# Optimization experiments

Measured on AMD Instinct MI355X. Metric: run time of the kernel, lower is better.

Reference implementation:

```python
import jax, jax.numpy as jnp
import numpy as np
import math

N = 100000      # num vertices
M = 50000       # num hyperedges
NNZ = 800000    # incidence entries
F_IN = 128
NHID = 128
NCLS = 40
DEPTH = 4
ALPHA = 0.1     # restart_alpha
LAMDA = 0.5


def setup_inputs() -> dict:
    key = jax.random.key(0)
    ks = jax.random.split(key, 8)
    x = jax.random.normal(ks[0], (N, F_IN), jnp.float32)
    vertex = jax.random.randint(ks[1], (NNZ,), 0, N)
    edges = jax.random.randint(ks[2], (NNZ,), 0, M)
    s0 = 1.0 / np.sqrt(F_IN)
    sh = 1.0 / np.sqrt(NHID)
    W0 = jax.random.uniform(ks[3], (F_IN, NHID), jnp.float32, -s0, s0)
    b0 = jax.random.uniform(ks[4], (NHID,), jnp.float32, -s0, s0)
    Ws = jax.random.uniform(ks[5], (DEPTH, NHID, NHID), jnp.float32, -sh, sh)
    Wout = jax.random.uniform(ks[6], (NHID, NCLS), jnp.float32, -sh, sh)
    bout = jax.random.uniform(ks[7], (NCLS,), jnp.float32, -sh, sh)
    return {"x": x, "W0": W0, "b0": b0, "Ws": Ws, "Wout": Wout,
            "bout": bout, "vertex": vertex, "edges": edges}


def reference(x, W0, b0, Ws, Wout, bout, vertex, edges):
    ones = jnp.ones((NNZ, 1), x.dtype)
    cnt_e = jnp.maximum(jax.ops.segment_sum(ones, edges, num_segments=M), 1.0)
    cnt_v = jnp.maximum(jax.ops.segment_sum(ones, vertex, num_segments=N), 1.0)

    x = jax.nn.relu(x @ W0 + b0)
    x0 = x
    for i in range(DEPTH):
        beta = math.log(LAMDA / (i + 1) + 1.0)
        # vertex -> edge mean aggregation
        Xve = x[vertex]                                          # [NNZ, NHID]
        Xe = jax.ops.segment_sum(Xve, edges, num_segments=M) / cnt_e
        # edge -> vertex mean aggregation
        Xev = Xe[edges]                                          # [NNZ, NHID]
        Xv = jax.ops.segment_sum(Xev, vertex, num_segments=N) / cnt_v
        # L2 row-normalize with detached scale (use_norm=True)
        norm = jnp.linalg.norm(Xv, axis=1, keepdims=True)
        scale = jax.lax.stop_gradient(jnp.where(norm > 0, 1.0 / norm, 0.0))
        Xv = Xv * scale
        # alpha/beta residual blend (UniGCNII)
        Xi = (1.0 - ALPHA) * Xv + ALPHA * x0
        x = jax.nn.relu((1.0 - beta) * Xi + beta * (Xi @ Ws[i]))
    return x @ Wout + bout
```

## Files before the change

### kernel.cpp

```cpp
#include <hip/hip_runtime.h>

#define NV 100000
#define NE 50000
#define NNZ_C 800000
#define CAP_E 64
#define CAP_V 48
#define NB_E 391
#define NB_V 782
#define CAPB_E 2560
#define CAPB_V 1408
#define OVF_CAP 810000
#define T_ITEMS 4096
#define N_TILES ((NNZ_C + T_ITEMS - 1) / T_ITEMS)

typedef unsigned int uint32;
typedef unsigned short u16;
typedef u16 u16x8 __attribute__((ext_vector_type(8)));
typedef short short8 __attribute__((ext_vector_type(8)));
typedef float floatx16 __attribute__((ext_vector_type(16)));

__device__ __forceinline__ float bf2f(u16 h) {
  return __uint_as_float(((uint32)h) << 16);
}
__device__ __forceinline__ u16 f2bf(float f) {
  uint32 u = __float_as_uint(f);
  u += 0x7FFF + ((u >> 16) & 1);
  return (u16)(u >> 16);
}


__global__ void zero_misc(int* __restrict__ cur, int n,
                          u16* __restrict__ dummyX, u16* __restrict__ dummyXe) {
  int i = blockIdx.x * blockDim.x + threadIdx.x;
  if (i < n) cur[i] = 0;
  if (i < 128) { dummyX[i] = 0; dummyXe[i] = 0; }
}


__global__ __launch_bounds__(256) void scatter_binned(const int* __restrict__ vertex,
                                                      const int* __restrict__ edges,
                                                      int* __restrict__ curE,
                                                      int* __restrict__ curV,
                                                      int* __restrict__ ovfCnt,
                                                      uint32* __restrict__ pairE,
                                                      uint32* __restrict__ pairV,
                                                      uint2* __restrict__ ovfE,
                                                      uint2* __restrict__ ovfV) {
  __shared__ int histE[NB_E], baseE[NB_E];
  __shared__ int histV[NB_V], baseV[NB_V];
  int t = threadIdx.x;
  for (int tile = blockIdx.x; tile < N_TILES; tile += gridDim.x) {
    for (int b = t; b < NB_E; b += 256) histE[b] = 0;
    for (int b = t; b < NB_V; b += 256) histV[b] = 0;
    __syncthreads();
    int base = tile * T_ITEMS;
    int ev[16], vv[16], rE[16], rV[16];
    #pragma unroll
    for (int i = 0; i < 16; i++) {
      int k = base + t + i * 256;
      if (k < NNZ_C) {
        ev[i] = edges[k];
        vv[i] = vertex[k];
        rE[i] = atomicAdd(&histE[ev[i] >> 7], 1);
        rV[i] = atomicAdd(&histV[vv[i] >> 7], 1);
      }
    }
    __syncthreads();
    for (int b = t; b < NB_E; b += 256) {
      int h = histE[b];
      baseE[b] = h ? atomicAdd(&curE[b], h) : 0;
    }
    for (int b = t; b < NB_V; b += 256) {
      int h = histV[b];
      baseV[b] = h ? atomicAdd(&curV[b], h) : 0;
    }
    __syncthreads();
    #pragma unroll
    for (int i = 0; i < 16; i++) {
      int k = base + t + i * 256;
      if (k < NNZ_C) {
        uint32 e = (uint32)ev[i], v = (uint32)vv[i];
        uint32 pkE = ((e & 127u) << 25) | v;
        uint32 pkV = ((v & 127u) << 25) | e;
        int pE = baseE[e >> 7] + rE[i];
        if (pE < CAPB_E) pairE[(size_t)(e >> 7) * CAPB_E + pE] = pkE;
        else { int op = atomicAdd(&ovfCnt[0], 1); if (op < OVF_CAP) ovfE[op] = make_uint2(e >> 7, pkE); }
        int pV = baseV[v >> 7] + rV[i];
        if (pV < CAPB_V) pairV[(size_t)(v >> 7) * CAPB_V + pV] = pkV;
        else { int op = atomicAdd(&ovfCnt[1], 1); if (op < OVF_CAP) ovfV[op] = make_uint2(v >> 7, pkV); }
      }
    }
    __syncthreads();
  }
}

__global__ __launch_bounds__(256) void expand(const uint32* __restrict__ pairs,
                                              const int* __restrict__ cur, int capb,
                                              const uint2* __restrict__ ovf,
                                              const int* __restrict__ ovfCnt,
                                              int* __restrict__ items, int cap,
                                              int* __restrict__ cnt, int nKeys,
                                              int P, int dummy) {
  __shared__ int lcnt[128];
  int b = blockIdx.x, t = threadIdx.x;
  if (t < 128) lcnt[t] = 0;
  __syncthreads();
  int n = min(cur[b], capb);
  const uint32* p = pairs + (size_t)b * capb;
  for (int i = t; i < n; i += 256) {
    uint32 w = p[i];
    int loc = w >> 25;
    int val = (int)(w & 0x1FFFFFFu);
    int r = atomicAdd(&lcnt[loc], 1);
    if (r < cap) items[(size_t)((b << 7) + loc) * cap + r] = val;
  }
  int novf = min(*ovfCnt, OVF_CAP);
  for (int i = t; i < novf; i += 256) {
    uint2 w = ovf[i];
    if ((int)w.x == b) {
      int loc = w.y >> 25;
      int val = (int)(w.y & 0x1FFFFFFu);
      int r = atomicAdd(&lcnt[loc], 1);
      if (r < cap) items[(size_t)((b << 7) + loc) * cap + r] = val;
    }
  }
  __syncthreads();
  if (t < 128) {
    int key = (b << 7) + t;
    if (key < nKeys) {
      int c = lcnt[t];
      cnt[key] = c;
      int cc = min(c, cap);
      int padded = min((cc + P - 1) & ~(P - 1), cap);
      for (int r = cc; r < padded; r++)
        items[(size_t)key * cap + r] = dummy;
    }
  }
}


__global__ void prep_weights(const float* __restrict__ W0, const float* __restrict__ Ws,
                             u16* __restrict__ WT) {
  int idx = blockIdx.x * blockDim.x + threadIdx.x;
  if (idx >= 5 * 16384) return;
  const float betas[4] = {0.4054651081f, 0.2231435513f, 0.1541506798f, 0.1177830357f};
  int sec = idx >> 14;
  int rc = idx & 16383;
  int n = rc >> 7, k = rc & 127;
  float v;
  if (sec == 0) {
    v = W0[k * 128 + n];
  } else {
    int i = sec - 1;
    float b = betas[i];
    v = b * Ws[i * 16384 + k * 128 + n];
    if (k == n) v += 1.0f - b;
  }
  WT[idx] = f2bf(v);
}


__global__ __launch_bounds__(256) void edge_agg(const u16* __restrict__ Xh,
                                                const int* __restrict__ cntE,
                                                const int* __restrict__ itemsE,
                                                u16* __restrict__ Xeh) {
  int g = threadIdx.x >> 4;
  int lane = threadIdx.x & 15;
  int e = blockIdx.x * 16 + g;
  int cnt = cntE[e];
  int n16 = (min(cnt, CAP_E) + 15) & ~15;
  const int* it = itemsE + (size_t)e * CAP_E;
  float acc[8] = {0.f, 0.f, 0.f, 0.f, 0.f, 0.f, 0.f, 0.f};
  for (int j = 0; j < n16; j += 16) {
    int4 i0 = *(const int4*)(it + j);
    int4 i1 = *(const int4*)(it + j + 4);
    int4 i2 = *(const int4*)(it + j + 8);
    int4 i3 = *(const int4*)(it + j + 12);
    u16x8 r0 = *(const u16x8*)(Xh + (size_t)i0.x * 128 + lane * 8);
    u16x8 r1 = *(const u16x8*)(Xh + (size_t)i0.y * 128 + lane * 8);
    u16x8 r2 = *(const u16x8*)(Xh + (size_t)i0.z * 128 + lane * 8);
    u16x8 r3 = *(const u16x8*)(Xh + (size_t)i0.w * 128 + lane * 8);
    u16x8 r4 = *(const u16x8*)(Xh + (size_t)i1.x * 128 + lane * 8);
    u16x8 r5 = *(const u16x8*)(Xh + (size_t)i1.y * 128 + lane * 8);
    u16x8 r6 = *(const u16x8*)(Xh + (size_t)i1.z * 128 + lane * 8);
    u16x8 r7 = *(const u16x8*)(Xh + (size_t)i1.w * 128 + lane * 8);
    u16x8 r8 = *(const u16x8*)(Xh + (size_t)i2.x * 128 + lane * 8);
    u16x8 r9 = *(const u16x8*)(Xh + (size_t)i2.y * 128 + lane * 8);
    u16x8 rA = *(const u16x8*)(Xh + (size_t)i2.z * 128 + lane * 8);
    u16x8 rB = *(const u16x8*)(Xh + (size_t)i2.w * 128 + lane * 8);
    u16x8 rC = *(const u16x8*)(Xh + (size_t)i3.x * 128 + lane * 8);
    u16x8 rD = *(const u16x8*)(Xh + (size_t)i3.y * 128 + lane * 8);
    u16x8 rE = *(const u16x8*)(Xh + (size_t)i3.z * 128 + lane * 8);
    u16x8 rF = *(const u16x8*)(Xh + (size_t)i3.w * 128 + lane * 8);
    #pragma unroll
    for (int q = 0; q < 8; q++) {
      float s0 = (bf2f(r0[q]) + bf2f(r1[q])) + (bf2f(r2[q]) + bf2f(r3[q]));
      float s1 = (bf2f(r4[q]) + bf2f(r5[q])) + (bf2f(r6[q]) + bf2f(r7[q]));
      float s2 = (bf2f(r8[q]) + bf2f(r9[q])) + (bf2f(rA[q]) + bf2f(rB[q]));
      float s3 = (bf2f(rC[q]) + bf2f(rD[q])) + (bf2f(rE[q]) + bf2f(rF[q]));
      acc[q] += (s0 + s1) + (s2 + s3);
    }
  }
  float inv = 1.f / fmaxf((float)cnt, 1.f);
  u16x8 o;
  #pragma unroll
  for (int q = 0; q < 8; q++) o[q] = f2bf(acc[q] * inv);
  *(u16x8*)(Xeh + (size_t)e * 128 + lane * 8) = o;
}

__global__ __launch_bounds__(256) void vertex_agg(const u16* __restrict__ Xeh,
                                                  const int* __restrict__ cntV,
                                                  const int* __restrict__ itemsV,
                                                  const u16* __restrict__ x0h,
                                                  u16* __restrict__ Xih) {
  int g = threadIdx.x >> 4;
  int lane = threadIdx.x & 15;
  int v = blockIdx.x * 16 + g;
  int cnt = cntV[v];
  int n8 = (min(cnt, CAP_V) + 7) & ~7;
  const int* it = itemsV + (size_t)v * CAP_V;
  u16x8 x0v = *(const u16x8*)(x0h + (size_t)v * 128 + lane * 8);
  float acc[8] = {0.f, 0.f, 0.f, 0.f, 0.f, 0.f, 0.f, 0.f};
  for (int j = 0; j < n8; j += 8) {
    int4 e0 = *(const int4*)(it + j);
    int4 e1 = *(const int4*)(it + j + 4);
    u16x8 r0 = *(const u16x8*)(Xeh + (size_t)e0.x * 128 + lane * 8);
    u16x8 r1 = *(const u16x8*)(Xeh + (size_t)e0.y * 128 + lane * 8);
    u16x8 r2 = *(const u16x8*)(Xeh + (size_t)e0.z * 128 + lane * 8);
    u16x8 r3 = *(const u16x8*)(Xeh + (size_t)e0.w * 128 + lane * 8);
    u16x8 r4 = *(const u16x8*)(Xeh + (size_t)e1.x * 128 + lane * 8);
    u16x8 r5 = *(const u16x8*)(Xeh + (size_t)e1.y * 128 + lane * 8);
    u16x8 r6 = *(const u16x8*)(Xeh + (size_t)e1.z * 128 + lane * 8);
    u16x8 r7 = *(const u16x8*)(Xeh + (size_t)e1.w * 128 + lane * 8);
    #pragma unroll
    for (int q = 0; q < 8; q++)
      acc[q] += ((bf2f(r0[q]) + bf2f(r1[q])) + (bf2f(r2[q]) + bf2f(r3[q]))) +
                ((bf2f(r4[q]) + bf2f(r5[q])) + (bf2f(r6[q]) + bf2f(r7[q])));
  }
  float inv = 1.f / fmaxf((float)cnt, 1.f);
  float sq = 0.f;
  #pragma unroll
  for (int q = 0; q < 8; q++) { acc[q] *= inv; sq += acc[q] * acc[q]; }
  sq += __shfl_xor(sq, 1, 64);
  sq += __shfl_xor(sq, 2, 64);
  sq += __shfl_xor(sq, 4, 64);
  sq += __shfl_xor(sq, 8, 64);
  float scale = (sq > 0.f) ? rsqrtf(sq) : 0.f;
  u16x8 o;
  #pragma unroll
  for (int q = 0; q < 8; q++)
    o[q] = f2bf(0.9f * acc[q] * scale + 0.1f * bf2f(x0v[q]));
  *(u16x8*)(Xih + (size_t)v * 128 + lane * 8) = o;
}


__global__ __launch_bounds__(256, 4) void gemm_mfma(const u16* __restrict__ Ah,
                                                    const u16* __restrict__ WT,
                                                    u16* __restrict__ Yh, int nrows) {
  __shared__ u16 As[128 * 136];
  int t = threadIdx.x;
  int row0 = blockIdx.x * 128;
  #pragma unroll
  for (int i = 0; i < 8; i++) {
    int idx = t + 256 * i;
    int r = idx >> 4, c8 = idx & 15;
    u16x8 v = {0, 0, 0, 0, 0, 0, 0, 0};
    if (row0 + r < nrows) v = *(const u16x8*)(Ah + (size_t)(row0 + r) * 128 + c8 * 8);
    *(u16x8*)&As[r * 136 + c8 * 8] = v;
  }
  __syncthreads();

  int w = t >> 6, lane = t & 63;
  int l31 = lane & 31, kh = lane >> 5;
  int wr = w >> 1, wc = w & 1;
  floatx16 acc[2][2];
  #pragma unroll
  for (int rt = 0; rt < 2; rt++)
    #pragma unroll
    for (int ct = 0; ct < 2; ct++)
      #pragma unroll
      for (int q = 0; q < 16; q++) acc[rt][ct][q] = 0.f;

  const u16* wtb0 = WT + (size_t)(wc * 64 + l31) * 128;
  const u16* wtb1 = WT + (size_t)(wc * 64 + 32 + l31) * 128;
  #pragma unroll
  for (int ks = 0; ks < 8; ks++) {
    int koff = ks * 16 + kh * 8;
    short8 b0 = *(const short8*)(wtb0 + koff);
    short8 b1 = *(const short8*)(wtb1 + koff);
    short8 a0 = *(const short8*)&As[(wr * 64 + l31) * 136 + koff];
    short8 a1 = *(const short8*)&As[(wr * 64 + 32 + l31) * 136 + koff];
    acc[0][0] = __builtin_amdgcn_mfma_f32_32x32x16_bf16(a0, b0, acc[0][0], 0, 0, 0);
    acc[0][1] = __builtin_amdgcn_mfma_f32_32x32x16_bf16(a0, b1, acc[0][1], 0, 0, 0);
    acc[1][0] = __builtin_amdgcn_mfma_f32_32x32x16_bf16(a1, b0, acc[1][0], 0, 0, 0);
    acc[1][1] = __builtin_amdgcn_mfma_f32_32x32x16_bf16(a1, b1, acc[1][1], 0, 0, 0);
  }
  __syncthreads();

  #pragma unroll
  for (int rt = 0; rt < 2; rt++)
    #pragma unroll
    for (int ct = 0; ct < 2; ct++) {
      int col = wc * 64 + ct * 32 + l31;
      #pragma unroll
      for (int reg = 0; reg < 16; reg++) {
        int row = wr * 64 + rt * 32 + (reg & 3) + 8 * (reg >> 2) + 4 * kh;
        As[row * 136 + col] = f2bf(fmaxf(acc[rt][ct][reg], 0.f));
      }
    }
  __syncthreads();
  #pragma unroll
  for (int i = 0; i < 8; i++) {
    int idx = t + 256 * i;
    int r = idx >> 4, c8 = idx & 15;
    if (row0 + r < nrows)
      *(u16x8*)(Yh + (size_t)(row0 + r) * 128 + c8 * 8) =
          *(const u16x8*)&As[r * 136 + c8 * 8];
  }
}

__global__ __launch_bounds__(256, 4) void gemm_first(const float* __restrict__ A,
                                                     const u16* __restrict__ WT,
                                                     const float* __restrict__ bias,
                                                     u16* __restrict__ Yh,
                                                     u16* __restrict__ Y2h, int nrows) {
  __shared__ u16 As[128 * 136];
  int t = threadIdx.x;
  int row0 = blockIdx.x * 128;
  #pragma unroll
  for (int i = 0; i < 8; i++) {
    int idx = t + 256 * i;
    int r = idx >> 4, c8 = idx & 15;
    u16x8 v = {0, 0, 0, 0, 0, 0, 0, 0};
    if (row0 + r < nrows) {
      const float* p = A + (size_t)(row0 + r) * 128 + c8 * 8;
      float4 a = *(const float4*)p;
      float4 b = *(const float4*)(p + 4);
      v[0] = f2bf(a.x); v[1] = f2bf(a.y); v[2] = f2bf(a.z); v[3] = f2bf(a.w);
      v[4] = f2bf(b.x); v[5] = f2bf(b.y); v[6] = f2bf(b.z); v[7] = f2bf(b.w);
    }
    *(u16x8*)&As[r * 136 + c8 * 8] = v;
  }
  __syncthreads();

  int w = t >> 6, lane = t & 63;
  int l31 = lane & 31, kh = lane >> 5;
  int wr = w >> 1, wc = w & 1;
  floatx16 acc[2][2];
  #pragma unroll
  for (int rt = 0; rt < 2; rt++)
    #pragma unroll
    for (int ct = 0; ct < 2; ct++)
      #pragma unroll
      for (int q = 0; q < 16; q++) acc[rt][ct][q] = 0.f;

  const u16* wtb0 = WT + (size_t)(wc * 64 + l31) * 128;
  const u16* wtb1 = WT + (size_t)(wc * 64 + 32 + l31) * 128;
  #pragma unroll
  for (int ks = 0; ks < 8; ks++) {
    int koff = ks * 16 + kh * 8;
    short8 b0 = *(const short8*)(wtb0 + koff);
    short8 b1 = *(const short8*)(wtb1 + koff);
    short8 a0 = *(const short8*)&As[(wr * 64 + l31) * 136 + koff];
    short8 a1 = *(const short8*)&As[(wr * 64 + 32 + l31) * 136 + koff];
    acc[0][0] = __builtin_amdgcn_mfma_f32_32x32x16_bf16(a0, b0, acc[0][0], 0, 0, 0);
    acc[0][1] = __builtin_amdgcn_mfma_f32_32x32x16_bf16(a0, b1, acc[0][1], 0, 0, 0);
    acc[1][0] = __builtin_amdgcn_mfma_f32_32x32x16_bf16(a1, b0, acc[1][0], 0, 0, 0);
    acc[1][1] = __builtin_amdgcn_mfma_f32_32x32x16_bf16(a1, b1, acc[1][1], 0, 0, 0);
  }
  __syncthreads();

  #pragma unroll
  for (int rt = 0; rt < 2; rt++)
    #pragma unroll
    for (int ct = 0; ct < 2; ct++) {
      int col = wc * 64 + ct * 32 + l31;
      float bv = bias[col];
      #pragma unroll
      for (int reg = 0; reg < 16; reg++) {
        int row = wr * 64 + rt * 32 + (reg & 3) + 8 * (reg >> 2) + 4 * kh;
        As[row * 136 + col] = f2bf(fmaxf(acc[rt][ct][reg] + bv, 0.f));
      }
    }
  __syncthreads();
  #pragma unroll
  for (int i = 0; i < 8; i++) {
    int idx = t + 256 * i;
    int r = idx >> 4, c8 = idx & 15;
    if (row0 + r < nrows) {
      u16x8 v = *(const u16x8*)&As[r * 136 + c8 * 8];
      *(u16x8*)(Yh + (size_t)(row0 + r) * 128 + c8 * 8) = v;
      *(u16x8*)(Y2h + (size_t)(row0 + r) * 128 + c8 * 8) = v;
    }
  }
}


__global__ __launch_bounds__(256) void gemm_out(const u16* __restrict__ Xh,
                                                const float* __restrict__ W,
                                                const float* __restrict__ bias,
                                                float* __restrict__ Y, int nrows) {
  __shared__ float xs[128][36];
  __shared__ float ws[32][44];
  int t = threadIdx.x;
  int tr = t >> 3;
  int tc = t & 7;
  int row0 = blockIdx.x * 128;
  float acc[4][5];
  #pragma unroll
  for (int i = 0; i < 4; i++)
    #pragma unroll
    for (int j = 0; j < 5; j++) acc[i][j] = 0.f;

  for (int k0 = 0; k0 < 128; k0 += 32) {
    #pragma unroll
    for (int i = 0; i < 2; i++) {
      int idx = t + 256 * i;
      int r = idx >> 2, c8 = idx & 3;
      int gr = row0 + r;
      u16x8 v = {0, 0, 0, 0, 0, 0, 0, 0};
      if (gr < nrows) v = *(const u16x8*)(Xh + (size_t)gr * 128 + k0 + c8 * 8);
      #pragma unroll
      for (int q = 0; q < 8; q++) xs[r][c8 * 8 + q] = bf2f(v[q]);
    }
    #pragma unroll
    for (int i = 0; i < 5; i++) {
      int idx = t + 256 * i;
      int r = idx / 40, c = idx % 40;
      ws[r][c] = W[(k0 + r) * 40 + c];
    }
    __syncthreads();
    #pragma unroll
    for (int kk4 = 0; kk4 < 8; kk4++) {
      float4 xv[4];
      #pragma unroll
      for (int i = 0; i < 4; i++) xv[i] = *(const float4*)&xs[tr + 32 * i][kk4 * 4];
      #pragma unroll
      for (int q = 0; q < 4; q++) {
        int kk = kk4 * 4 + q;
        float wv[5];
        #pragma unroll
        for (int j = 0; j < 5; j++) wv[j] = ws[kk][tc * 5 + j];
        #pragma unroll
        for (int i = 0; i < 4; i++) {
          float xq = ((const float*)&xv[i])[q];
          #pragma unroll
          for (int j = 0; j < 5; j++) acc[i][j] += xq * wv[j];
        }
      }
    }
    __syncthreads();
  }
  #pragma unroll
  for (int i = 0; i < 4; i++) {
    int gr = row0 + tr + 32 * i;
    if (gr >= nrows) continue;
    #pragma unroll
    for (int j = 0; j < 5; j++) {
      int c = tc * 5 + j;
      Y[(long)gr * 40 + c] = acc[i][j] + bias[c];
    }
  }
}


extern "C" void kernel_launch(void* const* d_in, const int* in_sizes, int n_in,
                              void* d_out, int out_size, void* d_ws, size_t ws_size,
                              hipStream_t stream) {
  const float* x    = (const float*)d_in[0];
  const float* W0   = (const float*)d_in[1];
  const float* b0   = (const float*)d_in[2];
  const float* Ws   = (const float*)d_in[3];
  const float* Wout = (const float*)d_in[4];
  const float* bout = (const float*)d_in[5];
  const int* vertex = (const int*)d_in[6];
  const int* edges  = (const int*)d_in[7];
  float* out = (float*)d_out;

  char* base = (char*)d_ws;
  size_t o = 0;
  auto alloc = [&](size_t bytes) -> char* {
    char* r = base + o;
    o += (bytes + 255) & ~(size_t)255;
    return r;
  };
  u16* x_curh = (u16*)alloc((size_t)(NV + 1) * 128 * 2);
  u16* x0h    = (u16*)alloc((size_t)NV * 128 * 2);
  u16* Xeh    = (u16*)alloc((size_t)(NE + 1) * 128 * 2);
  u16* WT     = (u16*)alloc((size_t)5 * 16384 * 2);
  int* cntE   = (int*)alloc((size_t)NE * 4);
  int* cntV   = (int*)alloc((size_t)NV * 4);
  int* itemsE = (int*)alloc((size_t)NE * CAP_E * 4);
  int* itemsV = (int*)alloc((size_t)NV * CAP_V * 4);
  uint32* pairE = (uint32*)alloc((size_t)NB_E * CAPB_E * 4);
  uint32* pairV = (uint32*)alloc((size_t)NB_V * CAPB_V * 4);
  uint2* ovfE  = (uint2*)alloc((size_t)OVF_CAP * 8);
  uint2* ovfV  = (uint2*)alloc((size_t)OVF_CAP * 8);
  int* curAll = (int*)alloc((size_t)(NB_E + NB_V + 2) * 4);
  int* curE = curAll;
  int* curV = curAll + NB_E;
  int* ovfCnt = curAll + NB_E + NB_V;

  int nzero = NB_E + NB_V + 2;
  zero_misc<<<(nzero + 255) / 256, 256, 0, stream>>>(curAll, nzero,
                                                     x_curh + (size_t)NV * 128,
                                                     Xeh + (size_t)NE * 128);
  scatter_binned<<<N_TILES, 256, 0, stream>>>(vertex, edges, curE, curV, ovfCnt,
                                              pairE, pairV, ovfE, ovfV);
  expand<<<NB_E, 256, 0, stream>>>(pairE, curE, CAPB_E, ovfE, ovfCnt,
                                   itemsE, CAP_E, cntE, NE, 16, NV);
  expand<<<NB_V, 256, 0, stream>>>(pairV, curV, CAPB_V, ovfV, ovfCnt + 1,
                                   itemsV, CAP_V, cntV, NV, 8, NE);
  prep_weights<<<(5 * 16384 + 255) / 256, 256, 0, stream>>>(W0, Ws, WT);

  int gblocks = (NV + 127) / 128;
  gemm_first<<<gblocks, 256, 0, stream>>>(x, WT, b0, x_curh, x0h, NV);

  for (int i = 0; i < 4; i++) {
    edge_agg<<<NE / 16, 256, 0, stream>>>(x_curh, cntE, itemsE, Xeh);
    vertex_agg<<<NV / 16, 256, 0, stream>>>(Xeh, cntV, itemsV, x0h, x_curh);
    gemm_mfma<<<gblocks, 256, 0, stream>>>(x_curh, WT + (size_t)(1 + i) * 16384,
                                           x_curh, NV);
  }
  gemm_out<<<gblocks, 256, 0, stream>>>(x_curh, Wout, bout, out, NV);
}
```

Before: 495.9 us.

## Fuse vertex aggregation and normalization into the per-layer MFMA GEMM kernel

Merges the vertex_agg kernel into the layer GEMM. Each 64-row block now gathers the edge features for its vertices, applies mean, L2 normalization and the alpha blend in LDS, and then runs the bf16 MFMA matmul with ReLU. This drops the global write and re-read of the intermediate Xi and one kernel launch per layer. In exchange the GEMM tile shrinks from 128 to 64 rows, and the gather latency now sits in front of the MFMA phase inside each block.

```diff
diff --git a/kernel.cpp b/kernel.cpp
--- a/kernel.cpp
+++ b/kernel.cpp
@@ -208,78 +208,72 @@
   *(u16x8*)(Xeh + (size_t)e * 128 + lane * 8) = o;
 }
 
-__global__ __launch_bounds__(256) void vertex_agg(const u16* __restrict__ Xeh,
-                                                  const int* __restrict__ cntV,
-                                                  const int* __restrict__ itemsV,
-                                                  const u16* __restrict__ x0h,
-                                                  u16* __restrict__ Xih) {
-  int g = threadIdx.x >> 4;
-  int lane = threadIdx.x & 15;
-  int v = blockIdx.x * 16 + g;
-  int cnt = cntV[v];
-  int n8 = (min(cnt, CAP_V) + 7) & ~7;
-  const int* it = itemsV + (size_t)v * CAP_V;
-  u16x8 x0v = *(const u16x8*)(x0h + (size_t)v * 128 + lane * 8);
-  float acc[8] = {0.f, 0.f, 0.f, 0.f, 0.f, 0.f, 0.f, 0.f};
-  for (int j = 0; j < n8; j += 8) {
-    int4 e0 = *(const int4*)(it + j);
-    int4 e1 = *(const int4*)(it + j + 4);
-    u16x8 r0 = *(const u16x8*)(Xeh + (size_t)e0.x * 128 + lane * 8);
-    u16x8 r1 = *(const u16x8*)(Xeh + (size_t)e0.y * 128 + lane * 8);
-    u16x8 r2 = *(const u16x8*)(Xeh + (size_t)e0.z * 128 + lane * 8);
-    u16x8 r3 = *(const u16x8*)(Xeh + (size_t)e0.w * 128 + lane * 8);
-    u16x8 r4 = *(const u16x8*)(Xeh + (size_t)e1.x * 128 + lane * 8);
-    u16x8 r5 = *(const u16x8*)(Xeh + (size_t)e1.y * 128 + lane * 8);
-    u16x8 r6 = *(const u16x8*)(Xeh + (size_t)e1.z * 128 + lane * 8);
-    u16x8 r7 = *(const u16x8*)(Xeh + (size_t)e1.w * 128 + lane * 8);
-    #pragma unroll
-    for (int q = 0; q < 8; q++)
-      acc[q] += ((bf2f(r0[q]) + bf2f(r1[q])) + (bf2f(r2[q]) + bf2f(r3[q]))) +
-                ((bf2f(r4[q]) + bf2f(r5[q])) + (bf2f(r6[q]) + bf2f(r7[q])));
-  }
-  float inv = 1.f / fmaxf((float)cnt, 1.f);
-  float sq = 0.f;
-  #pragma unroll
-  for (int q = 0; q < 8; q++) { acc[q] *= inv; sq += acc[q] * acc[q]; }
-  sq += __shfl_xor(sq, 1, 64);
-  sq += __shfl_xor(sq, 2, 64);
-  sq += __shfl_xor(sq, 4, 64);
-  sq += __shfl_xor(sq, 8, 64);
-  float scale = (sq > 0.f) ? rsqrtf(sq) : 0.f;
-  u16x8 o;
-  #pragma unroll
-  for (int q = 0; q < 8; q++)
-    o[q] = f2bf(0.9f * acc[q] * scale + 0.1f * bf2f(x0v[q]));
-  *(u16x8*)(Xih + (size_t)v * 128 + lane * 8) = o;
-}
-
-
-__global__ __launch_bounds__(256, 4) void gemm_mfma(const u16* __restrict__ Ah,
-                                                    const u16* __restrict__ WT,
-                                                    u16* __restrict__ Yh, int nrows) {
-  __shared__ u16 As[128 * 136];
+
+__global__ __launch_bounds__(256, 5) void gemm_fused(const u16* __restrict__ Xeh,
+                                                     const int* __restrict__ cntV,
+                                                     const int* __restrict__ itemsV,
+                                                     const u16* __restrict__ x0h,
+                                                     const u16* __restrict__ WT,
+                                                     u16* __restrict__ Yh, int nrows) {
+  __shared__ u16 As[64 * 136];
   int t = threadIdx.x;
-  int row0 = blockIdx.x * 128;
-  #pragma unroll
-  for (int i = 0; i < 8; i++) {
-    int idx = t + 256 * i;
-    int r = idx >> 4, c8 = idx & 15;
-    u16x8 v = {0, 0, 0, 0, 0, 0, 0, 0};
-    if (row0 + r < nrows) v = *(const u16x8*)(Ah + (size_t)(row0 + r) * 128 + c8 * 8);
-    *(u16x8*)&As[r * 136 + c8 * 8] = v;
-  }
-  __syncthreads();
-
-  int w = t >> 6, lane = t & 63;
-  int l31 = lane & 31, kh = lane >> 5;
+  int row0 = blockIdx.x * 64;
+  int g = t >> 4, lane = t & 15;
+  #pragma unroll
+  for (int pass = 0; pass < 4; pass++) {
+    int r = pass * 16 + g;
+    int v = row0 + r;
+    float acc[8] = {0.f, 0.f, 0.f, 0.f, 0.f, 0.f, 0.f, 0.f};
+    int cnt = 0;
+    if (v < nrows) {
+      cnt = cntV[v];
+      int n8 = (min(cnt, CAP_V) + 7) & ~7;
+      const int* it = itemsV + (size_t)v * CAP_V;
+      for (int j = 0; j < n8; j += 8) {
+        int4 e0 = *(const int4*)(it + j);
+        int4 e1 = *(const int4*)(it + j + 4);
+        u16x8 r0 = *(const u16x8*)(Xeh + (size_t)e0.x * 128 + lane * 8);
+        u16x8 r1 = *(const u16x8*)(Xeh + (size_t)e0.y * 128 + lane * 8);
+        u16x8 r2 = *(const u16x8*)(Xeh + (size_t)e0.z * 128 + lane * 8);
+        u16x8 r3 = *(const u16x8*)(Xeh + (size_t)e0.w * 128 + lane * 8);
+        u16x8 r4 = *(const u16x8*)(Xeh + (size_t)e1.x * 128 + lane * 8);
+        u16x8 r5 = *(const u16x8*)(Xeh + (size_t)e1.y * 128 + lane * 8);
+        u16x8 r6 = *(const u16x8*)(Xeh + (size_t)e1.z * 128 + lane * 8);
+        u16x8 r7 = *(const u16x8*)(Xeh + (size_t)e1.w * 128 + lane * 8);
+        #pragma unroll
+        for (int q = 0; q < 8; q++)
+          acc[q] += ((bf2f(r0[q]) + bf2f(r1[q])) + (bf2f(r2[q]) + bf2f(r3[q]))) +
+                    ((bf2f(r4[q]) + bf2f(r5[q])) + (bf2f(r6[q]) + bf2f(r7[q])));
+      }
+    }
+    float inv = 1.f / fmaxf((float)cnt, 1.f);
+    float sq = 0.f;
+    #pragma unroll
+    for (int q = 0; q < 8; q++) { acc[q] *= inv; sq += acc[q] * acc[q]; }
+    sq += __shfl_xor(sq, 1, 64);
+    sq += __shfl_xor(sq, 2, 64);
+    sq += __shfl_xor(sq, 4, 64);
+    sq += __shfl_xor(sq, 8, 64);
+    float scale = (sq > 0.f) ? rsqrtf(sq) : 0.f;
+    u16x8 o = {0, 0, 0, 0, 0, 0, 0, 0};
+    if (v < nrows) {
+      u16x8 x0v = *(const u16x8*)(x0h + (size_t)v * 128 + lane * 8);
+      #pragma unroll
+      for (int q = 0; q < 8; q++)
+        o[q] = f2bf(0.9f * acc[q] * scale + 0.1f * bf2f(x0v[q]));
+    }
+    *(u16x8*)&As[r * 136 + lane * 8] = o;
+  }
+  __syncthreads();
+
+  int w = t >> 6, lane64 = t & 63;
+  int l31 = lane64 & 31, kh = lane64 >> 5;
   int wr = w >> 1, wc = w & 1;
-  floatx16 acc[2][2];
-  #pragma unroll
-  for (int rt = 0; rt < 2; rt++)
-    #pragma unroll
-    for (int ct = 0; ct < 2; ct++)
-      #pragma unroll
-      for (int q = 0; q < 16; q++) acc[rt][ct][q] = 0.f;
+  floatx16 acc[2];
+  #pragma unroll
+  for (int ct = 0; ct < 2; ct++)
+    #pragma unroll
+    for (int q = 0; q < 16; q++) acc[ct][q] = 0.f;
 
   const u16* wtb0 = WT + (size_t)(wc * 64 + l31) * 128;
   const u16* wtb1 = WT + (size_t)(wc * 64 + 32 + l31) * 128;
@@ -288,29 +282,24 @@
     int koff = ks * 16 + kh * 8;
     short8 b0 = *(const short8*)(wtb0 + koff);
     short8 b1 = *(const short8*)(wtb1 + koff);
-    short8 a0 = *(const short8*)&As[(wr * 64 + l31) * 136 + koff];
-    short8 a1 = *(const short8*)&As[(wr * 64 + 32 + l31) * 136 + koff];
-    acc[0][0] = __builtin_amdgcn_mfma_f32_32x32x16_bf16(a0, b0, acc[0][0], 0, 0, 0);
-    acc[0][1] = __builtin_amdgcn_mfma_f32_32x32x16_bf16(a0, b1, acc[0][1], 0, 0, 0);
-    acc[1][0] = __builtin_amdgcn_mfma_f32_32x32x16_bf16(a1, b0, acc[1][0], 0, 0, 0);
-    acc[1][1] = __builtin_amdgcn_mfma_f32_32x32x16_bf16(a1, b1, acc[1][1], 0, 0, 0);
-  }
-  __syncthreads();
-
-  #pragma unroll
-  for (int rt = 0; rt < 2; rt++)
-    #pragma unroll
-    for (int ct = 0; ct < 2; ct++) {
-      int col = wc * 64 + ct * 32 + l31;
-      #pragma unroll
-      for (int reg = 0; reg < 16; reg++) {
-        int row = wr * 64 + rt * 32 + (reg & 3) + 8 * (reg >> 2) + 4 * kh;
-        As[row * 136 + col] = f2bf(fmaxf(acc[rt][ct][reg], 0.f));
-      }
-    }
-  __syncthreads();
-  #pragma unroll
-  for (int i = 0; i < 8; i++) {
+    short8 a0 = *(const short8*)&As[(wr * 32 + l31) * 136 + koff];
+    acc[0] = __builtin_amdgcn_mfma_f32_32x32x16_bf16(a0, b0, acc[0], 0, 0, 0);
+    acc[1] = __builtin_amdgcn_mfma_f32_32x32x16_bf16(a0, b1, acc[1], 0, 0, 0);
+  }
+  __syncthreads();
+
+  #pragma unroll
+  for (int ct = 0; ct < 2; ct++) {
+    int col = wc * 64 + ct * 32 + l31;
+    #pragma unroll
+    for (int reg = 0; reg < 16; reg++) {
+      int row = wr * 32 + (reg & 3) + 8 * (reg >> 2) + 4 * kh;
+      As[row * 136 + col] = f2bf(fmaxf(acc[ct][reg], 0.f));
+    }
+  }
+  __syncthreads();
+  #pragma unroll
+  for (int i = 0; i < 4; i++) {
     int idx = t + 256 * i;
     int r = idx >> 4, c8 = idx & 15;
     if (row0 + r < nrows)
@@ -514,13 +503,13 @@
   prep_weights<<<(5 * 16384 + 255) / 256, 256, 0, stream>>>(W0, Ws, WT);
 
   int gblocks = (NV + 127) / 128;
+  int fblocks = (NV + 63) / 64;
   gemm_first<<<gblocks, 256, 0, stream>>>(x, WT, b0, x_curh, x0h, NV);
 
   for (int i = 0; i < 4; i++) {
     edge_agg<<<NE / 16, 256, 0, stream>>>(x_curh, cntE, itemsE, Xeh);
-    vertex_agg<<<NV / 16, 256, 0, stream>>>(Xeh, cntV, itemsV, x0h, x_curh);
-    gemm_mfma<<<gblocks, 256, 0, stream>>>(x_curh, WT + (size_t)(1 + i) * 16384,
-                                           x_curh, NV);
+    gemm_fused<<<fblocks, 256, 0, stream>>>(Xeh, cntV, itemsV, x0h,
+                                            WT + (size_t)(1 + i) * 16384, x_curh, NV);
   }
   gemm_out<<<gblocks, 256, 0, stream>>>(x_curh, Wout, bout, out, NV);
 }
```

Result: faster. 481.0 us, median of 2 (-3.0%).
